# Kernel tuning notes

Measured on AMD Instinct MI355X. Metric: run time of the kernel, lower is better.

The kernel has to match this reference:

```python
import jax, jax.numpy as jnp
import numpy as np

NU, NI, D, E = 50000, 100000, 128, 500000
UMAX, IMAX = 50, 50
SQRT_D = float(np.sqrt(D))


def seg_softmax(vals, seg, n):
    # numerically stable softmax over edges grouped by segment id (sparse row softmax)
    m = jax.ops.segment_max(vals, seg, num_segments=n)
    ex = jnp.exp(vals - m[seg])
    s = jax.ops.segment_sum(ex, seg, num_segments=n)
    return ex / s[seg]


def setup_inputs() -> dict:
    key = jax.random.key(0)
    ks = jax.random.split(key, 20)
    w = lambda k: jax.random.normal(k, (D, D), dtype=jnp.float32) * 0.05
    return {
        "u_emb": jax.random.normal(ks[0], (NU, D), dtype=jnp.float32),
        "i_emb": jax.random.normal(ks[1], (NI, D), dtype=jnp.float32),
        "edge_u": jax.random.randint(ks[2], (E,), 0, NU),
        "edge_i": jax.random.randint(ks[3], (E,), 0, NI),
        "rui": jax.random.randint(ks[4], (E,), 0, UMAX),
        "riu": jax.random.randint(ks[5], (E,), 0, IMAX),
        "last_u_items": jax.random.randint(ks[6], (NU,), 0, NI),
        "last_i_users": jax.random.randint(ks[7], (NU,), 0, NU),
        "W1": w(ks[8]), "W2": w(ks[9]), "W1b": w(ks[10]), "W2b": w(ks[11]),
        "W3": w(ks[12]), "W4": w(ks[13]),
        "pV": jax.random.normal(ks[14], (UMAX, D), dtype=jnp.float32),
        "pK": jax.random.normal(ks[15], (IMAX, D), dtype=jnp.float32),
        "last_user_table": jax.random.normal(ks[16], (NU, D), dtype=jnp.float32),
        "last_item_table": jax.random.normal(ks[17], (NI, D), dtype=jnp.float32),
    }


def reference(u_emb, i_emb, edge_u, edge_i, rui, riu, last_u_items, last_i_users,
              W1, W2, W1b, W2b, W3, W4, pV, pK, last_user_table, last_item_table):
    # nn.Linear: y = x @ W.T
    um = u_emb @ W2.T            # (NU, D) user messages
    im = i_emb @ W1.T            # (NI, D) item messages
    um_e = um[edge_u]            # (E, D) gathered per edge
    im_e = im[edge_i]            # (E, D)

    # ---- long term ----
    # dense e = um @ im.T masked to edges == per-edge dot products (same math)
    e_vals = jnp.sum(um_e * im_e, axis=-1)                     # (E,)
    pVui = pV[rui]                                             # (E, D)
    pKiu = pK[riu]                                             # (E, D)
    e_ui = e_vals + jnp.sum(um_e * pVui, axis=-1)
    e_iu = e_vals + jnp.sum(im_e * pKiu, axis=-1)
    alphas = seg_softmax(e_ui / SQRT_D, edge_u, NU)            # softmax over items per user
    betas = seg_softmax(e_iu / SQRT_D, edge_i, NI)             # softmax over users per item

    umb = u_emb @ W2b.T
    imb = i_emb @ W1b.T
    # pass_messages: out[row] = sum_e alpha_e * (messages[col_e] + p_e)
    hLu = jax.ops.segment_sum(alphas[:, None] * (imb[edge_i] + pKiu), edge_u, num_segments=NU)
    hLi = jax.ops.segment_sum(betas[:, None] * (umb[edge_u] + pVui), edge_i, num_segments=NI)

    # ---- short term ----
    li = last_item_table[last_u_items] @ W3.T                  # (NU, D)
    lu = last_user_table[last_i_users] @ W4.T                  # (NU, D)
    a_vals = jnp.sum(li[edge_u] * im_e, axis=-1)               # (E,)
    b_vals = jnp.sum(lu[edge_u] * im_e, axis=-1)               # (E,)
    alphas_s = seg_softmax(a_vals / SQRT_D, edge_u, NU)
    betas_s = seg_softmax(b_vals / SQRT_D, edge_i, NI)
    # p = ones -> messages + 1
    hSu = jax.ops.segment_sum(alphas_s[:, None] * (im_e + 1.0), edge_u, num_segments=NU)
    hSi = jax.ops.segment_sum(betas_s[:, None] * (um_e + 1.0), edge_i, num_segments=NI)

    return (hLu, hSu, hLi, hSi)
```

## Files before the change

### kernel.cpp

```cpp
#include <hip/hip_runtime.h>
#include <hip/hip_bf16.h>
#include <math.h>

#define D_ 128
#define INV_SQRT_D 0.08838834764831845f
#define SCAN_CH 16
#define SCAN_TILE (256 * SCAN_CH)

typedef __bf16 bf16x8 __attribute__((ext_vector_type(8)));
typedef float f32x4 __attribute__((ext_vector_type(4)));

struct W6 { const float* p[6]; };

__device__ __forceinline__ void unpack8(bf16x8 v, float* f) {
    const uint32_t* u = (const uint32_t*)&v;
#pragma unroll
    for (int i = 0; i < 4; i++) {
        uint32_t w = u[i];
        f[2 * i]     = __uint_as_float(w << 16);
        f[2 * i + 1] = __uint_as_float(w & 0xffff0000u);
    }
}

__global__ __launch_bounds__(256) void cvt_weights(W6 w, __bf16* __restrict__ out) {
    int idx = blockIdx.x * 256 + threadIdx.x;
    if (idx >= 6 * 16384) return;
    out[idx] = (__bf16)w.p[idx >> 14][idx & 16383];
}

__global__ __launch_bounds__(256) void cvt2(const float* __restrict__ a, const float* __restrict__ b,
                                            __bf16* __restrict__ oa, __bf16* __restrict__ ob, int n) {
    int idx = blockIdx.x * 256 + threadIdx.x;
    if (idx < n) { oa[idx] = (__bf16)a[idx]; ob[idx] = (__bf16)b[idx]; }
}

__global__ __launch_bounds__(256) void gemm_xwt(const float* __restrict__ X,
                                                const int* __restrict__ gidx,
                                                const __bf16* __restrict__ Wb,
                                                __bf16* __restrict__ Y, int ystride, int rows) {
    int lane = threadIdx.x & 63;
    int wave = threadIdx.x >> 6;
    int row0 = blockIdx.x * 64 + wave * 16;
    if (row0 >= rows) return;
    int l16 = lane & 15, kh = lane >> 4;
    int ar = row0 + l16;
    int arc = ar < rows ? ar : rows - 1;
    long srcrow = gidx ? (long)gidx[arc] : (long)arc;
    const float* arow = X + (size_t)srcrow * D_;

    f32x4 acc[8] = {};
#pragma unroll
    for (int k0 = 0; k0 < D_; k0 += 32) {
        int kk = k0 + kh * 8;
        float4 a0 = *(const float4*)(arow + kk);
        float4 a1 = *(const float4*)(arow + kk + 4);
        bf16x8 af;
        af[0] = (__bf16)a0.x; af[1] = (__bf16)a0.y; af[2] = (__bf16)a0.z; af[3] = (__bf16)a0.w;
        af[4] = (__bf16)a1.x; af[5] = (__bf16)a1.y; af[6] = (__bf16)a1.z; af[7] = (__bf16)a1.w;
#pragma unroll
        for (int cb = 0; cb < 8; cb++) {
            bf16x8 bf = *(const bf16x8*)(Wb + (size_t)(cb * 16 + l16) * D_ + kk);
            acc[cb] = __builtin_amdgcn_mfma_f32_16x16x32_bf16(af, bf, acc[cb], 0, 0, 0);
        }
    }
#pragma unroll
    for (int cb = 0; cb < 8; cb++) {
#pragma unroll
        for (int j = 0; j < 4; j++) {
            int r = row0 + kh * 4 + j;
            if (r < rows) Y[(size_t)r * ystride + cb * 16 + l16] = (__bf16)acc[cb][j];
        }
    }
}

__global__ __launch_bounds__(256) void gemm_dual(const float* __restrict__ X,
                                                 const __bf16* __restrict__ WA,
                                                 const __bf16* __restrict__ WB,
                                                 __bf16* __restrict__ YA, int sA,
                                                 __bf16* __restrict__ YB, int sB, int rows) {
    int lane = threadIdx.x & 63;
    int wave = threadIdx.x >> 6;
    int row0 = blockIdx.x * 64 + wave * 16;
    if (row0 >= rows) return;
    int l16 = lane & 15, kh = lane >> 4;
    int ar = row0 + l16;
    int arc = ar < rows ? ar : rows - 1;
    const float* arow = X + (size_t)arc * D_;

    f32x4 accA[8] = {}, accB[8] = {};
#pragma unroll
    for (int k0 = 0; k0 < D_; k0 += 32) {
        int kk = k0 + kh * 8;
        float4 a0 = *(const float4*)(arow + kk);
        float4 a1 = *(const float4*)(arow + kk + 4);
        bf16x8 af;
        af[0] = (__bf16)a0.x; af[1] = (__bf16)a0.y; af[2] = (__bf16)a0.z; af[3] = (__bf16)a0.w;
        af[4] = (__bf16)a1.x; af[5] = (__bf16)a1.y; af[6] = (__bf16)a1.z; af[7] = (__bf16)a1.w;
#pragma unroll
        for (int cb = 0; cb < 8; cb++) {
            bf16x8 bfA = *(const bf16x8*)(WA + (size_t)(cb * 16 + l16) * D_ + kk);
            accA[cb] = __builtin_amdgcn_mfma_f32_16x16x32_bf16(af, bfA, accA[cb], 0, 0, 0);
            bf16x8 bfB = *(const bf16x8*)(WB + (size_t)(cb * 16 + l16) * D_ + kk);
            accB[cb] = __builtin_amdgcn_mfma_f32_16x16x32_bf16(af, bfB, accB[cb], 0, 0, 0);
        }
    }
#pragma unroll
    for (int cb = 0; cb < 8; cb++) {
#pragma unroll
        for (int j = 0; j < 4; j++) {
            int r = row0 + kh * 4 + j;
            if (r < rows) {
                YA[(size_t)r * sA + cb * 16 + l16] = (__bf16)accA[cb][j];
                YB[(size_t)r * sB + cb * 16 + l16] = (__bf16)accB[cb][j];
            }
        }
    }
}

__global__ __launch_bounds__(256) void gemm_pvk(const __bf16* __restrict__ Xb, int xstride,
                                                const __bf16* __restrict__ Pb,
                                                float* __restrict__ Y, int rows, int ncols) {
    int lane = threadIdx.x & 63;
    int wave = threadIdx.x >> 6;
    int row0 = blockIdx.x * 64 + wave * 16;
    if (row0 >= rows) return;
    int l16 = lane & 15, kh = lane >> 4;
    int ar = row0 + l16;
    int arc = ar < rows ? ar : rows - 1;
    const __bf16* arow = Xb + (size_t)arc * xstride;

    f32x4 acc[4] = {};
#pragma unroll
    for (int k0 = 0; k0 < D_; k0 += 32) {
        int kk = k0 + kh * 8;
        bf16x8 af = *(const bf16x8*)(arow + kk);
#pragma unroll
        for (int cb = 0; cb < 4; cb++) {
            int br = cb * 16 + l16;
            if (br >= ncols) br = ncols - 1;
            bf16x8 bf = *(const bf16x8*)(Pb + (size_t)br * D_ + kk);
            acc[cb] = __builtin_amdgcn_mfma_f32_16x16x32_bf16(af, bf, acc[cb], 0, 0, 0);
        }
    }
#pragma unroll
    for (int cb = 0; cb < 4; cb++) {
        int col = cb * 16 + l16;
        if (col >= ncols) continue;
#pragma unroll
        for (int j = 0; j < 4; j++) {
            int r = row0 + kh * 4 + j;
            if (r < rows) Y[(size_t)r * ncols + col] = acc[cb][j] * INV_SQRT_D;
        }
    }
}

__global__ __launch_bounds__(256) void hist2(const int* __restrict__ eu, const int* __restrict__ ei,
                                             int* __restrict__ cnt_all, int nu, int E) {
    int e = blockIdx.x * 256 + threadIdx.x;
    if (e < E) {
        atomicAdd(&cnt_all[eu[e]], 1);
        atomicAdd(&cnt_all[nu + ei[e]], 1);
    }
}

__global__ __launch_bounds__(256) void scan_phaseA(const int* __restrict__ cnt, int* __restrict__ part, int n) {
    __shared__ int wsum[4];
    int t = threadIdx.x, lane = t & 63, w = t >> 6;
    int i0 = blockIdx.x * SCAN_TILE + t * SCAN_CH;
    int tot = 0;
#pragma unroll
    for (int j = 0; j < SCAN_CH; j++) tot += (i0 + j < n) ? cnt[i0 + j] : 0;
#pragma unroll
    for (int d = 32; d; d >>= 1) tot += __shfl_xor(tot, d);
    if (lane == 0) wsum[w] = tot;
    __syncthreads();
    if (t == 0) part[blockIdx.x] = wsum[0] + wsum[1] + wsum[2] + wsum[3];
}

__global__ __launch_bounds__(1024) void scan_phaseB(int* __restrict__ part, int nb,
                                                    int* __restrict__ off, int n) {
    __shared__ int wsum[16];
    int t = threadIdx.x, lane = t & 63, w = t >> 6;
    int v = (t < nb) ? part[t] : 0;
    int x = v;
#pragma unroll
    for (int d = 1; d < 64; d <<= 1) {
        int y = __shfl_up(x, d);
        if (lane >= d) x += y;
    }
    if (lane == 63) wsum[w] = x;
    __syncthreads();
    int wbase = 0;
    for (int ww = 0; ww < w; ww++) wbase += wsum[ww];
    if (t < nb) part[t] = wbase + x - v;
    if (t == 1023) off[n] = wbase + x;
}

__global__ __launch_bounds__(256) void scan_phaseC(const int* __restrict__ cnt, const int* __restrict__ part,
                                                   int* __restrict__ off, int* __restrict__ pos, int n) {
    __shared__ int wsum[4];
    int t = threadIdx.x, lane = t & 63, w = t >> 6;
    int i0 = blockIdx.x * SCAN_TILE + t * SCAN_CH;
    int loc[SCAN_CH];
    int tot = 0;
#pragma unroll
    for (int j = 0; j < SCAN_CH; j++) {
        int v = (i0 + j < n) ? cnt[i0 + j] : 0;
        loc[j] = tot; tot += v;
    }
    int x = tot;
#pragma unroll
    for (int d = 1; d < 64; d <<= 1) {
        int y = __shfl_up(x, d);
        if (lane >= d) x += y;
    }
    if (lane == 63) wsum[w] = x;
    __syncthreads();
    int wbase = 0;
    for (int ww = 0; ww < w; ww++) wbase += wsum[ww];
    int excl = part[blockIdx.x] + wbase + x - tot;
#pragma unroll
    for (int j = 0; j < SCAN_CH; j++) {
        if (i0 + j < n) { off[i0 + j] = excl + loc[j]; pos[i0 + j] = excl + loc[j]; }
    }
}

__global__ __launch_bounds__(256) void scatter2(const int* __restrict__ eu, const int* __restrict__ ei,
                                                int* __restrict__ pos_all, int* __restrict__ list_all,
                                                int nu, int E) {
    int e = blockIdx.x * 256 + threadIdx.x;
    if (e < E) {
        int pu = atomicAdd(&pos_all[eu[e]], 1);
        list_all[pu] = e;
        int pi = atomicAdd(&pos_all[nu + ei[e]], 1);
        list_all[pi] = e;
    }
}

__global__ __launch_bounds__(256) void user_fused(const int* __restrict__ off_all, const int* __restrict__ list_all,
                                                  const int* __restrict__ ei, const int* __restrict__ rui,
                                                  const int* __restrict__ riu,
                                                  const __bf16* __restrict__ i_rec,
                                                  const __bf16* __restrict__ u_rec,
                                                  const __bf16* __restrict__ li_t,
                                                  const __bf16* __restrict__ lu_t,
                                                  const __bf16* __restrict__ pKb,
                                                  const float* __restrict__ upv,
                                                  float2* __restrict__ mb_val,
                                                  float* __restrict__ hLu, float* __restrict__ hSu,
                                                  int nu, int umax) {
    int u = blockIdx.x * 4 + (threadIdx.x >> 6);
    if (u >= nu) return;
    int lane = threadIdx.x & 63;
    int g = lane >> 4, l16 = lane & 15;
    int off = off_all[u], n = off_all[u + 1] - off;
    if (n == 0) {
        if (lane < 16) {
            float4 z = make_float4(0.f, 0.f, 0.f, 0.f);
            ((float4*)(hLu + (size_t)u * D_ + l16 * 8))[0] = z;
            ((float4*)(hLu + (size_t)u * D_ + l16 * 8))[1] = z;
            ((float4*)(hSu + (size_t)u * D_ + l16 * 8))[0] = z;
            ((float4*)(hSu + (size_t)u * D_ + l16 * 8))[1] = z;
        }
        return;
    }
    float um8[8], li8[8], lu8[8];
    unpack8(((const bf16x8*)(u_rec + (size_t)u * 256))[l16], um8);
    unpack8(((const bf16x8*)(li_t + (size_t)u * D_))[l16], li8);
    unpack8(((const bf16x8*)(lu_t + (size_t)u * D_))[l16], lu8);
#pragma unroll
    for (int j = 0; j < 8; j++) { um8[j] *= INV_SQRT_D; li8[j] *= INV_SQRT_D; lu8[j] *= INV_SQRT_D; }
    const float* upv_row = upv + (size_t)u * umax;

    float s1 = 0.f, s2 = 0.f, a1[8] = {}, a2[8] = {};
    for (int i = g; i < n; i += 4) {
        int e = list_all[off + i];
        int item = ei[e];
        const __bf16* ib = i_rec + (size_t)item * 256;
        bf16x8 imv  = ((const bf16x8*)ib)[l16];
        bf16x8 imbv = ((const bf16x8*)(ib + 128))[l16];
        bf16x8 pkv  = ((const bf16x8*)(pKb + (size_t)riu[e] * D_))[l16];
        float fim[8], fimb[8], fpk[8];
        unpack8(imv, fim); unpack8(imbv, fimb); unpack8(pkv, fpk);
        float d1 = 0.f, d2 = 0.f, d3 = 0.f;
#pragma unroll
        for (int j = 0; j < 8; j++) {
            d1 = fmaf(um8[j], fim[j], d1);
            d2 = fmaf(li8[j], fim[j], d2);
            d3 = fmaf(lu8[j], fim[j], d3);
        }
#pragma unroll
        for (int d = 1; d < 16; d <<= 1) {
            d1 += __shfl_xor(d1, d);
            d2 += __shfl_xor(d2, d);
            d3 += __shfl_xor(d3, d);
        }
        if (l16 == 0) mb_val[e] = make_float2(d1, d3);
        float w1 = __expf(d1 + upv_row[rui[e]]);
        float w2 = __expf(d2);
        s1 += w1; s2 += w2;
#pragma unroll
        for (int j = 0; j < 8; j++) {
            a1[j] = fmaf(w1, fimb[j] + fpk[j], a1[j]);
            a2[j] = fmaf(w2, fim[j], a2[j]);
        }
    }
#pragma unroll
    for (int d = 16; d < 64; d <<= 1) {
        s1 += __shfl_xor(s1, d); s2 += __shfl_xor(s2, d);
#pragma unroll
        for (int j = 0; j < 8; j++) {
            a1[j] += __shfl_xor(a1[j], d);
            a2[j] += __shfl_xor(a2[j], d);
        }
    }
    if (lane < 16) {
        float inv1 = 1.f / s1, inv2 = 1.f / s2;
        ((float4*)(hLu + (size_t)u * D_ + l16 * 8))[0] = make_float4(a1[0]*inv1, a1[1]*inv1, a1[2]*inv1, a1[3]*inv1);
        ((float4*)(hLu + (size_t)u * D_ + l16 * 8))[1] = make_float4(a1[4]*inv1, a1[5]*inv1, a1[6]*inv1, a1[7]*inv1);
        ((float4*)(hSu + (size_t)u * D_ + l16 * 8))[0] = make_float4(a2[0]*inv2+1.f, a2[1]*inv2+1.f, a2[2]*inv2+1.f, a2[3]*inv2+1.f);
        ((float4*)(hSu + (size_t)u * D_ + l16 * 8))[1] = make_float4(a2[4]*inv2+1.f, a2[5]*inv2+1.f, a2[6]*inv2+1.f, a2[7]*inv2+1.f);
    }
}

__global__ __launch_bounds__(256) void item_fused(const int* __restrict__ off_all, const int* __restrict__ list_all,
                                                  const int* __restrict__ eu, const int* __restrict__ rui,
                                                  const int* __restrict__ riu,
                                                  const __bf16* __restrict__ u_rec,
                                                  const __bf16* __restrict__ pVb,
                                                  const float* __restrict__ ipk,
                                                  const float2* __restrict__ mb_val,
                                                  float* __restrict__ hLi, float* __restrict__ hSi,
                                                  int nu, int ni, int imax) {
    int it = blockIdx.x * 4 + (threadIdx.x >> 6);
    if (it >= ni) return;
    int lane = threadIdx.x & 63;
    int g = lane >> 4, l16 = lane & 15;
    int off = off_all[nu + it], n = off_all[nu + it + 1] - off;
    if (n == 0) {
        if (lane < 16) {
            float4 z = make_float4(0.f, 0.f, 0.f, 0.f);
            ((float4*)(hLi + (size_t)it * D_ + l16 * 8))[0] = z;
            ((float4*)(hLi + (size_t)it * D_ + l16 * 8))[1] = z;
            ((float4*)(hSi + (size_t)it * D_ + l16 * 8))[0] = z;
            ((float4*)(hSi + (size_t)it * D_ + l16 * 8))[1] = z;
        }
        return;
    }
    const float* ipk_row = ipk + (size_t)it * imax;

    float s1 = 0.f, s2 = 0.f, a1[8] = {}, a2[8] = {};
    for (int i = g; i < n; i += 4) {
        int e = list_all[off + i];
        int user = eu[e];
        float2 mb = mb_val[e];
        const __bf16* ub = u_rec + (size_t)user * 256;
        bf16x8 umv  = ((const bf16x8*)ub)[l16];
        bf16x8 umbv = ((const bf16x8*)(ub + 128))[l16];
        bf16x8 pvv  = ((const bf16x8*)(pVb + (size_t)rui[e] * D_))[l16];
        float fum[8], fumb[8], fpv[8];
        unpack8(umv, fum); unpack8(umbv, fumb); unpack8(pvv, fpv);
        float w1 = __expf(mb.x + ipk_row[riu[e]]);
        float w2 = __expf(mb.y);
        s1 += w1; s2 += w2;
#pragma unroll
        for (int j = 0; j < 8; j++) {
            a1[j] = fmaf(w1, fumb[j] + fpv[j], a1[j]);
            a2[j] = fmaf(w2, fum[j], a2[j]);
        }
    }
#pragma unroll
    for (int d = 16; d < 64; d <<= 1) {
        s1 += __shfl_xor(s1, d); s2 += __shfl_xor(s2, d);
#pragma unroll
        for (int j = 0; j < 8; j++) {
            a1[j] += __shfl_xor(a1[j], d);
            a2[j] += __shfl_xor(a2[j], d);
        }
    }
    if (lane < 16) {
        float inv1 = 1.f / s1, inv2 = 1.f / s2;
        ((float4*)(hLi + (size_t)it * D_ + l16 * 8))[0] = make_float4(a1[0]*inv1, a1[1]*inv1, a1[2]*inv1, a1[3]*inv1);
        ((float4*)(hLi + (size_t)it * D_ + l16 * 8))[1] = make_float4(a1[4]*inv1, a1[5]*inv1, a1[6]*inv1, a1[7]*inv1);
        ((float4*)(hSi + (size_t)it * D_ + l16 * 8))[0] = make_float4(a2[0]*inv2+1.f, a2[1]*inv2+1.f, a2[2]*inv2+1.f, a2[3]*inv2+1.f);
        ((float4*)(hSi + (size_t)it * D_ + l16 * 8))[1] = make_float4(a2[4]*inv2+1.f, a2[5]*inv2+1.f, a2[6]*inv2+1.f, a2[7]*inv2+1.f);
    }
}

extern "C" void kernel_launch(void* const* d_in, const int* in_sizes, int n_in,
                              void* d_out, int out_size, void* d_ws, size_t ws_size,
                              hipStream_t stream) {
    (void)n_in; (void)out_size; (void)ws_size;
    const float* u_emb = (const float*)d_in[0];
    const float* i_emb = (const float*)d_in[1];
    const int* edge_u = (const int*)d_in[2];
    const int* edge_i = (const int*)d_in[3];
    const int* rui = (const int*)d_in[4];
    const int* riu = (const int*)d_in[5];
    const int* last_u_items = (const int*)d_in[6];
    const int* last_i_users = (const int*)d_in[7];
    const float* W1  = (const float*)d_in[8];
    const float* W2  = (const float*)d_in[9];
    const float* W1b = (const float*)d_in[10];
    const float* W2b = (const float*)d_in[11];
    const float* W3  = (const float*)d_in[12];
    const float* W4  = (const float*)d_in[13];
    const float* pV  = (const float*)d_in[14];
    const float* pK  = (const float*)d_in[15];
    const float* last_user_table = (const float*)d_in[16];
    const float* last_item_table = (const float*)d_in[17];

    const int NU = in_sizes[0] / D_;
    const int NI = in_sizes[1] / D_;
    const int E  = in_sizes[2];
    const int UMAXr = in_sizes[14] / D_;
    const int IMAXr = in_sizes[15] / D_;
    const int NSEG = NU + NI;

    size_t cur = 0;
    auto alloc = [&](size_t bytes) -> void* {
        void* p = (char*)d_ws + cur;
        cur += (bytes + 255) & ~(size_t)255;
        return p;
    };

    __bf16* Wb    = (__bf16*)alloc(6 * 16384 * sizeof(__bf16));
    __bf16* pVb   = (__bf16*)alloc((size_t)UMAXr * D_ * 2);
    __bf16* pKb   = (__bf16*)alloc((size_t)IMAXr * D_ * 2);
    __bf16* i_rec = (__bf16*)alloc((size_t)NI * 256 * 2);
    __bf16* u_rec = (__bf16*)alloc((size_t)NU * 256 * 2);
    __bf16* li_bf = (__bf16*)alloc((size_t)NU * D_ * 2);
    __bf16* lu_bf = (__bf16*)alloc((size_t)NU * D_ * 2);
    float* upv    = (float*)alloc((size_t)NU * UMAXr * 4);
    float* ipk    = (float*)alloc((size_t)NI * IMAXr * 4);
    float2* mb_val = (float2*)alloc((size_t)E * 8);
    int* cnt_all  = (int*)alloc((size_t)NSEG * 4);
    int* off_all  = (int*)alloc((size_t)(NSEG + 1) * 4);
    int* pos_all  = (int*)alloc((size_t)NSEG * 4);
    int* list_all = (int*)alloc((size_t)2 * E * 4);
    int* parts    = (int*)alloc(1024 * 4);

    float* out = (float*)d_out;
    float* hLu = out;
    float* hSu = out + (size_t)NU * D_;
    float* hLi = out + (size_t)2 * NU * D_;
    float* hSi = out + (size_t)2 * NU * D_ + (size_t)NI * D_;

    W6 w6;
    w6.p[0] = W1; w6.p[1] = W2; w6.p[2] = W1b; w6.p[3] = W2b; w6.p[4] = W3; w6.p[5] = W4;
    cvt_weights<<<(6 * 16384 + 255) / 256, 256, 0, stream>>>(w6, Wb);
    cvt2<<<(UMAXr * D_ + 255) / 256, 256, 0, stream>>>(pV, pK, pVb, pKb, UMAXr * D_);

    hipMemsetAsync(cnt_all, 0, (size_t)NSEG * 4, stream);
    hist2<<<(E + 255) / 256, 256, 0, stream>>>(edge_u, edge_i, cnt_all, NU, E);
    int nb = (NSEG + SCAN_TILE - 1) / SCAN_TILE;
    scan_phaseA<<<nb, 256, 0, stream>>>(cnt_all, parts, NSEG);
    scan_phaseB<<<1, 1024, 0, stream>>>(parts, nb, off_all, NSEG);
    scan_phaseC<<<nb, 256, 0, stream>>>(cnt_all, parts, off_all, pos_all, NSEG);
    scatter2<<<(E + 255) / 256, 256, 0, stream>>>(edge_u, edge_i, pos_all, list_all, NU, E);

    int gu = (NU + 63) / 64, gi = (NI + 63) / 64;
    gemm_dual<<<gi, 256, 0, stream>>>(i_emb, Wb + 0 * 16384, Wb + 2 * 16384,
                                      i_rec + 0, 256, i_rec + 128, 256, NI);
    gemm_dual<<<gu, 256, 0, stream>>>(u_emb, Wb + 1 * 16384, Wb + 3 * 16384,
                                      u_rec + 0, 256, u_rec + 128, 256, NU);
    gemm_xwt<<<gu, 256, 0, stream>>>(last_item_table, last_u_items, Wb + 4 * 16384, li_bf, 128, NU);
    gemm_xwt<<<gu, 256, 0, stream>>>(last_user_table, last_i_users, Wb + 5 * 16384, lu_bf, 128, NU);

    gemm_pvk<<<gu, 256, 0, stream>>>(u_rec, 256, pVb, upv, NU, UMAXr);
    gemm_pvk<<<gi, 256, 0, stream>>>(i_rec, 256, pKb, ipk, NI, IMAXr);

    user_fused<<<(NU + 3) / 4, 256, 0, stream>>>(off_all, list_all, edge_i, rui, riu,
                                                 i_rec, u_rec, li_bf, lu_bf, pKb, upv, mb_val,
                                                 hLu, hSu, NU, UMAXr);
    item_fused<<<(NI + 3) / 4, 256, 0, stream>>>(off_all, list_all, edge_u, rui, riu,
                                                 u_rec, pVb, ipk, mb_val,
                                                 hLi, hSi, NU, NI, IMAXr);
}
```

Before: 495.5 us.

## Scatter packed edge records into CSR order and unroll segment loops by two

The scatter pass now writes packed int4 records per CSR slot (neighbour id, both relation indices, and the item-side slot). The fused user and item kernels read these directly instead of chasing list→edge→attribute indirections. mb_val is now indexed by item-CSR position, so the item kernel reads it contiguously. Both edge loops process two edges per iteration to expose more independent gathers, and the two short-term GEMMs are merged into one launch. The cost is a larger record buffer, more registers per thread, and bigger scatter writes.

```diff
diff --git a/kernel.cpp b/kernel.cpp
--- a/kernel.cpp
+++ b/kernel.cpp
@@ -32,45 +32,6 @@
                                             __bf16* __restrict__ oa, __bf16* __restrict__ ob, int n) {
     int idx = blockIdx.x * 256 + threadIdx.x;
     if (idx < n) { oa[idx] = (__bf16)a[idx]; ob[idx] = (__bf16)b[idx]; }
-}
-
-__global__ __launch_bounds__(256) void gemm_xwt(const float* __restrict__ X,
-                                                const int* __restrict__ gidx,
-                                                const __bf16* __restrict__ Wb,
-                                                __bf16* __restrict__ Y, int ystride, int rows) {
-    int lane = threadIdx.x & 63;
-    int wave = threadIdx.x >> 6;
-    int row0 = blockIdx.x * 64 + wave * 16;
-    if (row0 >= rows) return;
-    int l16 = lane & 15, kh = lane >> 4;
-    int ar = row0 + l16;
-    int arc = ar < rows ? ar : rows - 1;
-    long srcrow = gidx ? (long)gidx[arc] : (long)arc;
-    const float* arow = X + (size_t)srcrow * D_;
-
-    f32x4 acc[8] = {};
-#pragma unroll
-    for (int k0 = 0; k0 < D_; k0 += 32) {
-        int kk = k0 + kh * 8;
-        float4 a0 = *(const float4*)(arow + kk);
-        float4 a1 = *(const float4*)(arow + kk + 4);
-        bf16x8 af;
-        af[0] = (__bf16)a0.x; af[1] = (__bf16)a0.y; af[2] = (__bf16)a0.z; af[3] = (__bf16)a0.w;
-        af[4] = (__bf16)a1.x; af[5] = (__bf16)a1.y; af[6] = (__bf16)a1.z; af[7] = (__bf16)a1.w;
-#pragma unroll
-        for (int cb = 0; cb < 8; cb++) {
-            bf16x8 bf = *(const bf16x8*)(Wb + (size_t)(cb * 16 + l16) * D_ + kk);
-            acc[cb] = __builtin_amdgcn_mfma_f32_16x16x32_bf16(af, bf, acc[cb], 0, 0, 0);
-        }
-    }
-#pragma unroll
-    for (int cb = 0; cb < 8; cb++) {
-#pragma unroll
-        for (int j = 0; j < 4; j++) {
-            int r = row0 + kh * 4 + j;
-            if (r < rows) Y[(size_t)r * ystride + cb * 16 + l16] = (__bf16)acc[cb][j];
-        }
-    }
 }
 
 __global__ __launch_bounds__(256) void gemm_dual(const float* __restrict__ X,
@@ -117,6 +78,54 @@
     }
 }
 
+__global__ __launch_bounds__(256) void gemm_lilu(const float* __restrict__ Xi, const int* __restrict__ gi_,
+                                                 const float* __restrict__ Xu, const int* __restrict__ gu_,
+                                                 const __bf16* __restrict__ Wli, const __bf16* __restrict__ Wlu,
+                                                 __bf16* __restrict__ Yli, __bf16* __restrict__ Ylu, int rows) {
+    int lane = threadIdx.x & 63;
+    int wave = threadIdx.x >> 6;
+    int row0 = blockIdx.x * 64 + wave * 16;
+    if (row0 >= rows) return;
+    int l16 = lane & 15, kh = lane >> 4;
+    int ar = row0 + l16;
+    int arc = ar < rows ? ar : rows - 1;
+    const float* arowA = Xi + (size_t)gi_[arc] * D_;
+    const float* arowB = Xu + (size_t)gu_[arc] * D_;
+
+    f32x4 accA[8] = {}, accB[8] = {};
+#pragma unroll
+    for (int k0 = 0; k0 < D_; k0 += 32) {
+        int kk = k0 + kh * 8;
+        float4 a0 = *(const float4*)(arowA + kk);
+        float4 a1 = *(const float4*)(arowA + kk + 4);
+        float4 b0 = *(const float4*)(arowB + kk);
+        float4 b1 = *(const float4*)(arowB + kk + 4);
+        bf16x8 afA, afB;
+        afA[0] = (__bf16)a0.x; afA[1] = (__bf16)a0.y; afA[2] = (__bf16)a0.z; afA[3] = (__bf16)a0.w;
+        afA[4] = (__bf16)a1.x; afA[5] = (__bf16)a1.y; afA[6] = (__bf16)a1.z; afA[7] = (__bf16)a1.w;
+        afB[0] = (__bf16)b0.x; afB[1] = (__bf16)b0.y; afB[2] = (__bf16)b0.z; afB[3] = (__bf16)b0.w;
+        afB[4] = (__bf16)b1.x; afB[5] = (__bf16)b1.y; afB[6] = (__bf16)b1.z; afB[7] = (__bf16)b1.w;
+#pragma unroll
+        for (int cb = 0; cb < 8; cb++) {
+            bf16x8 bfA = *(const bf16x8*)(Wli + (size_t)(cb * 16 + l16) * D_ + kk);
+            accA[cb] = __builtin_amdgcn_mfma_f32_16x16x32_bf16(afA, bfA, accA[cb], 0, 0, 0);
+            bf16x8 bfB = *(const bf16x8*)(Wlu + (size_t)(cb * 16 + l16) * D_ + kk);
+            accB[cb] = __builtin_amdgcn_mfma_f32_16x16x32_bf16(afB, bfB, accB[cb], 0, 0, 0);
+        }
+    }
+#pragma unroll
+    for (int cb = 0; cb < 8; cb++) {
+#pragma unroll
+        for (int j = 0; j < 4; j++) {
+            int r = row0 + kh * 4 + j;
+            if (r < rows) {
+                Yli[(size_t)r * D_ + cb * 16 + l16] = (__bf16)accA[cb][j];
+                Ylu[(size_t)r * D_ + cb * 16 + l16] = (__bf16)accB[cb][j];
+            }
+        }
+    }
+}
+
 __global__ __launch_bounds__(256) void gemm_pvk(const __bf16* __restrict__ Xb, int xstride,
                                                 const __bf16* __restrict__ Pb,
                                                 float* __restrict__ Y, int rows, int ncols) {
@@ -226,20 +235,20 @@
 }
 
 __global__ __launch_bounds__(256) void scatter2(const int* __restrict__ eu, const int* __restrict__ ei,
-                                                int* __restrict__ pos_all, int* __restrict__ list_all,
+                                                const int* __restrict__ rui, const int* __restrict__ riu,
+                                                int* __restrict__ pos_all, int4* __restrict__ recs,
                                                 int nu, int E) {
     int e = blockIdx.x * 256 + threadIdx.x;
     if (e < E) {
-        int pu = atomicAdd(&pos_all[eu[e]], 1);
-        list_all[pu] = e;
-        int pi = atomicAdd(&pos_all[nu + ei[e]], 1);
-        list_all[pi] = e;
-    }
-}
-
-__global__ __launch_bounds__(256) void user_fused(const int* __restrict__ off_all, const int* __restrict__ list_all,
-                                                  const int* __restrict__ ei, const int* __restrict__ rui,
-                                                  const int* __restrict__ riu,
+        int u = eu[e], it = ei[e], r1 = rui[e], r2 = riu[e];
+        int pi = atomicAdd(&pos_all[nu + it], 1);
+        int pu = atomicAdd(&pos_all[u], 1);
+        recs[pu] = make_int4(it, r1, r2, pi);
+        recs[pi] = make_int4(u, r1, r2, 0);
+    }
+}
+
+__global__ __launch_bounds__(256) void user_fused(const int* __restrict__ off_all, const int4* __restrict__ recs,
                                                   const __bf16* __restrict__ i_rec,
                                                   const __bf16* __restrict__ u_rec,
                                                   const __bf16* __restrict__ li_t,
@@ -273,36 +282,49 @@
     const float* upv_row = upv + (size_t)u * umax;
 
     float s1 = 0.f, s2 = 0.f, a1[8] = {}, a2[8] = {};
-    for (int i = g; i < n; i += 4) {
-        int e = list_all[off + i];
-        int item = ei[e];
-        const __bf16* ib = i_rec + (size_t)item * 256;
-        bf16x8 imv  = ((const bf16x8*)ib)[l16];
-        bf16x8 imbv = ((const bf16x8*)(ib + 128))[l16];
-        bf16x8 pkv  = ((const bf16x8*)(pKb + (size_t)riu[e] * D_))[l16];
-        float fim[8], fimb[8], fpk[8];
-        unpack8(imv, fim); unpack8(imbv, fimb); unpack8(pkv, fpk);
-        float d1 = 0.f, d2 = 0.f, d3 = 0.f;
+    for (int i = g; i < n; i += 8) {
+        int4 ra = recs[off + i];
+        bool hb = (i + 4) < n;
+        int4 rb = recs[off + (hb ? i + 4 : i)];
+        const __bf16* pa = i_rec + (size_t)ra.x * 256;
+        const __bf16* pb = i_rec + (size_t)rb.x * 256;
+        bf16x8 vimA = ((const bf16x8*)pa)[l16];
+        bf16x8 vmbA = ((const bf16x8*)(pa + 128))[l16];
+        bf16x8 vpkA = ((const bf16x8*)(pKb + (size_t)ra.z * D_))[l16];
+        bf16x8 vimB = ((const bf16x8*)pb)[l16];
+        bf16x8 vmbB = ((const bf16x8*)(pb + 128))[l16];
+        bf16x8 vpkB = ((const bf16x8*)(pKb + (size_t)rb.z * D_))[l16];
+        float fimA[8], fmbA[8], fpkA[8], fimB[8], fmbB[8], fpkB[8];
+        unpack8(vimA, fimA); unpack8(vmbA, fmbA); unpack8(vpkA, fpkA);
+        unpack8(vimB, fimB); unpack8(vmbB, fmbB); unpack8(vpkB, fpkB);
+        float d1a = 0.f, d2a = 0.f, d3a = 0.f, d1b = 0.f, d2b = 0.f, d3b = 0.f;
 #pragma unroll
         for (int j = 0; j < 8; j++) {
-            d1 = fmaf(um8[j], fim[j], d1);
-            d2 = fmaf(li8[j], fim[j], d2);
-            d3 = fmaf(lu8[j], fim[j], d3);
+            d1a = fmaf(um8[j], fimA[j], d1a);
+            d2a = fmaf(li8[j], fimA[j], d2a);
+            d3a = fmaf(lu8[j], fimA[j], d3a);
+            d1b = fmaf(um8[j], fimB[j], d1b);
+            d2b = fmaf(li8[j], fimB[j], d2b);
+            d3b = fmaf(lu8[j], fimB[j], d3b);
         }
 #pragma unroll
         for (int d = 1; d < 16; d <<= 1) {
-            d1 += __shfl_xor(d1, d);
-            d2 += __shfl_xor(d2, d);
-            d3 += __shfl_xor(d3, d);
-        }
-        if (l16 == 0) mb_val[e] = make_float2(d1, d3);
-        float w1 = __expf(d1 + upv_row[rui[e]]);
-        float w2 = __expf(d2);
-        s1 += w1; s2 += w2;
+            d1a += __shfl_xor(d1a, d); d2a += __shfl_xor(d2a, d); d3a += __shfl_xor(d3a, d);
+            d1b += __shfl_xor(d1b, d); d2b += __shfl_xor(d2b, d); d3b += __shfl_xor(d3b, d);
+        }
+        if (l16 == 0) {
+            mb_val[ra.w] = make_float2(d1a, d3a);
+            if (hb) mb_val[rb.w] = make_float2(d1b, d3b);
+        }
+        float w1a = __expf(d1a + upv_row[ra.y]);
+        float w2a = __expf(d2a);
+        float w1b = hb ? __expf(d1b + upv_row[rb.y]) : 0.f;
+        float w2b = hb ? __expf(d2b) : 0.f;
+        s1 += w1a + w1b; s2 += w2a + w2b;
 #pragma unroll
         for (int j = 0; j < 8; j++) {
-            a1[j] = fmaf(w1, fimb[j] + fpk[j], a1[j]);
-            a2[j] = fmaf(w2, fim[j], a2[j]);
+            a1[j] = fmaf(w1a, fmbA[j] + fpkA[j], fmaf(w1b, fmbB[j] + fpkB[j], a1[j]));
+            a2[j] = fmaf(w2a, fimA[j], fmaf(w2b, fimB[j], a2[j]));
         }
     }
 #pragma unroll
@@ -323,9 +345,7 @@
     }
 }
 
-__global__ __launch_bounds__(256) void item_fused(const int* __restrict__ off_all, const int* __restrict__ list_all,
-                                                  const int* __restrict__ eu, const int* __restrict__ rui,
-                                                  const int* __restrict__ riu,
+__global__ __launch_bounds__(256) void item_fused(const int* __restrict__ off_all, const int4* __restrict__ recs,
                                                   const __bf16* __restrict__ u_rec,
                                                   const __bf16* __restrict__ pVb,
                                                   const float* __restrict__ ipk,
@@ -350,23 +370,32 @@
     const float* ipk_row = ipk + (size_t)it * imax;
 
     float s1 = 0.f, s2 = 0.f, a1[8] = {}, a2[8] = {};
-    for (int i = g; i < n; i += 4) {
-        int e = list_all[off + i];
-        int user = eu[e];
-        float2 mb = mb_val[e];
-        const __bf16* ub = u_rec + (size_t)user * 256;
-        bf16x8 umv  = ((const bf16x8*)ub)[l16];
-        bf16x8 umbv = ((const bf16x8*)(ub + 128))[l16];
-        bf16x8 pvv  = ((const bf16x8*)(pVb + (size_t)rui[e] * D_))[l16];
-        float fum[8], fumb[8], fpv[8];
-        unpack8(umv, fum); unpack8(umbv, fumb); unpack8(pvv, fpv);
-        float w1 = __expf(mb.x + ipk_row[riu[e]]);
-        float w2 = __expf(mb.y);
-        s1 += w1; s2 += w2;
+    for (int i = g; i < n; i += 8) {
+        int4 ra = recs[off + i];
+        bool hb = (i + 4) < n;
+        int4 rb = recs[off + (hb ? i + 4 : i)];
+        float2 ma = mb_val[off + i];
+        float2 mbv = hb ? mb_val[off + i + 4] : make_float2(0.f, 0.f);
+        const __bf16* pa = u_rec + (size_t)ra.x * 256;
+        const __bf16* pb = u_rec + (size_t)rb.x * 256;
+        bf16x8 vumA  = ((const bf16x8*)pa)[l16];
+        bf16x8 vmbA  = ((const bf16x8*)(pa + 128))[l16];
+        bf16x8 vpvA  = ((const bf16x8*)(pVb + (size_t)ra.y * D_))[l16];
+        bf16x8 vumB  = ((const bf16x8*)pb)[l16];
+        bf16x8 vmbB  = ((const bf16x8*)(pb + 128))[l16];
+        bf16x8 vpvB  = ((const bf16x8*)(pVb + (size_t)rb.y * D_))[l16];
+        float fumA[8], fmbA[8], fpvA[8], fumB[8], fmbB[8], fpvB[8];
+        unpack8(vumA, fumA); unpack8(vmbA, fmbA); unpack8(vpvA, fpvA);
+        unpack8(vumB, fumB); unpack8(vmbB, fmbB); unpack8(vpvB, fpvB);
+        float w1a = __expf(ma.x + ipk_row[ra.z]);
+        float w2a = __expf(ma.y);
+        float w1b = hb ? __expf(mbv.x + ipk_row[rb.z]) : 0.f;
+        float w2b = hb ? __expf(mbv.y) : 0.f;
+        s1 += w1a + w1b; s2 += w2a + w2b;
 #pragma unroll
         for (int j = 0; j < 8; j++) {
-            a1[j] = fmaf(w1, fumb[j] + fpv[j], a1[j]);
-            a2[j] = fmaf(w2, fum[j], a2[j]);
+            a1[j] = fmaf(w1a, fmbA[j] + fpvA[j], fmaf(w1b, fmbB[j] + fpvB[j], a1[j]));
+            a2[j] = fmaf(w2a, fumA[j], fmaf(w2b, fumB[j], a2[j]));
         }
     }
 #pragma unroll
@@ -433,11 +462,11 @@
     __bf16* lu_bf = (__bf16*)alloc((size_t)NU * D_ * 2);
     float* upv    = (float*)alloc((size_t)NU * UMAXr * 4);
     float* ipk    = (float*)alloc((size_t)NI * IMAXr * 4);
-    float2* mb_val = (float2*)alloc((size_t)E * 8);
+    float2* mb_val = (float2*)alloc((size_t)2 * E * 8);
+    int4* recs    = (int4*)alloc((size_t)2 * E * 16);
     int* cnt_all  = (int*)alloc((size_t)NSEG * 4);
     int* off_all  = (int*)alloc((size_t)(NSEG + 1) * 4);
     int* pos_all  = (int*)alloc((size_t)NSEG * 4);
-    int* list_all = (int*)alloc((size_t)2 * E * 4);
     int* parts    = (int*)alloc(1024 * 4);
 
     float* out = (float*)d_out;
@@ -457,23 +486,21 @@
     scan_phaseA<<<nb, 256, 0, stream>>>(cnt_all, parts, NSEG);
     scan_phaseB<<<1, 1024, 0, stream>>>(parts, nb, off_all, NSEG);
     scan_phaseC<<<nb, 256, 0, stream>>>(cnt_all, parts, off_all, pos_all, NSEG);
-    scatter2<<<(E + 255) / 256, 256, 0, stream>>>(edge_u, edge_i, pos_all, list_all, NU, E);
+    scatter2<<<(E + 255) / 256, 256, 0, stream>>>(edge_u, edge_i, rui, riu, pos_all, recs, NU, E);
 
     int gu = (NU + 63) / 64, gi = (NI + 63) / 64;
     gemm_dual<<<gi, 256, 0, stream>>>(i_emb, Wb + 0 * 16384, Wb + 2 * 16384,
                                       i_rec + 0, 256, i_rec + 128, 256, NI);
     gemm_dual<<<gu, 256, 0, stream>>>(u_emb, Wb + 1 * 16384, Wb + 3 * 16384,
                                       u_rec + 0, 256, u_rec + 128, 256, NU);
-    gemm_xwt<<<gu, 256, 0, stream>>>(last_item_table, last_u_items, Wb + 4 * 16384, li_bf, 128, NU);
-    gemm_xwt<<<gu, 256, 0, stream>>>(last_user_table, last_i_users, Wb + 5 * 16384, lu_bf, 128, NU);
+    gemm_lilu<<<gu, 256, 0, stream>>>(last_item_table, last_u_items, last_user_table, last_i_users,
+                                      Wb + 4 * 16384, Wb + 5 * 16384, li_bf, lu_bf, NU);
 
     gemm_pvk<<<gu, 256, 0, stream>>>(u_rec, 256, pVb, upv, NU, UMAXr);
     gemm_pvk<<<gi, 256, 0, stream>>>(i_rec, 256, pKb, ipk, NI, IMAXr);
 
-    user_fused<<<(NU + 3) / 4, 256, 0, stream>>>(off_all, list_all, edge_i, rui, riu,
-                                                 i_rec, u_rec, li_bf, lu_bf, pKb, upv, mb_val,
-                                                 hLu, hSu, NU, UMAXr);
-    item_fused<<<(NI + 3) / 4, 256, 0, stream>>>(off_all, list_all, edge_u, rui, riu,
-                                                 u_rec, pVb, ipk, mb_val,
+    user_fused<<<(NU + 3) / 4, 256, 0, stream>>>(off_all, recs, i_rec, u_rec, li_bf, lu_bf,
+                                                 pKb, upv, mb_val, hLu, hSu, NU, UMAXr);
+    item_fused<<<(NI + 3) / 4, 256, 0, stream>>>(off_all, recs, u_rec, pVb, ipk, mb_val,
                                                  hLi, hSi, NU, NI, IMAXr);
 }
```

After: 489.3 us. No clear change (-1.3%).
